# Performance work log

Hardware: AMD Instinct MI355X
Metric: run time of the kernel (lower is better)

The kernel has to match this reference:

```python
import jax, jax.numpy as jnp
import numpy as np

B = 1024
INPUT_DIM = 768
NUM_CLASSES = 5
NUM_PRIMARY_CAPS = 32
PRIMARY_CAP_DIM = 8
ROUTING_CAP_DIM = 16
NUM_ITER = 3
PROJ_DIM = 256 * 6 * 6  # 9216
NUM_IN_CAPS = NUM_PRIMARY_CAPS * 16  # conv output is 4x4 spatial -> 512


def squash(t, axis=-1):
    sq = jnp.sum(t * t, axis=axis, keepdims=True)
    scale = sq / (1.0 + sq)
    return scale * t / jnp.sqrt(sq + 1e-8)


def setup_inputs() -> dict:
    key = jax.random.key(0)
    k = jax.random.split(key, 6)
    x = jax.random.normal(k[0], (B, INPUT_DIM), dtype=jnp.float32)
    W1 = jax.random.normal(k[1], (INPUT_DIM, PROJ_DIM), dtype=jnp.float32) * 0.02
    b1 = jnp.zeros((PROJ_DIM,), dtype=jnp.float32)
    convW = jax.random.normal(k[2], (NUM_PRIMARY_CAPS * PRIMARY_CAP_DIM, 256, 3, 3), dtype=jnp.float32) * 0.02  # OIHW
    convB = jnp.zeros((NUM_PRIMARY_CAPS * PRIMARY_CAP_DIM,), dtype=jnp.float32)
    # matches torch.randn init in RoutingCapsules: [num_in, num_out, out_dim, in_dim]
    Wr = jax.random.normal(k[3], (NUM_IN_CAPS, NUM_CLASSES, ROUTING_CAP_DIM, PRIMARY_CAP_DIM), dtype=jnp.float32)
    return {"x": x, "W1": W1, "b1": b1, "convW": convW, "convB": convB, "Wr": Wr}


def reference(x, W1, b1, convW, convB, Wr):
    # feature projection (dropout is identity in eval)
    h = jax.nn.relu(x @ W1 + b1)
    h = h.reshape(-1, 256, 6, 6)
    # primary capsules conv: k=3, s=1, pad=0 -> [B, 256, 4, 4]
    out = jax.lax.conv_general_dilated(h, convW, window_strides=(1, 1), padding='VALID',
                                       dimension_numbers=('NCHW', 'OIHW', 'NCHW'))
    out = out + convB[None, :, None, None]
    bsz = out.shape[0]
    out = out.reshape(bsz, NUM_PRIMARY_CAPS, PRIMARY_CAP_DIM, -1)      # [B,32,8,16]
    out = jnp.transpose(out, (0, 1, 3, 2)).reshape(bsz, -1, PRIMARY_CAP_DIM)  # [B,512,8]
    u = squash(out, axis=-1)
    # prediction vectors u_hat: [B, in_caps, out_caps, out_dim]
    u_hat = jnp.einsum('nodi,bni->bnod', Wr, u)
    # dynamic routing
    b_logits = jnp.zeros((bsz, NUM_IN_CAPS, NUM_CLASSES, 1), dtype=u_hat.dtype)
    v = None
    for it in range(NUM_ITER):
        c = jax.nn.softmax(b_logits, axis=2)
        s = jnp.sum(c * u_hat, axis=1)  # [B, out_caps, out_dim]
        v = squash(s, axis=-1)
        if it < NUM_ITER - 1:
            agreement = jnp.sum(u_hat * v[:, None], axis=-1, keepdims=True)
            b_logits = b_logits + agreement
    class_probs = jnp.sqrt(jnp.sum(v * v, axis=-1))
    return (class_probs, v)
```

## Files before the change

### kernel.cpp

```cpp
#include <hip/hip_runtime.h>
#include <hip/hip_fp16.h>

#define BSZ   1024
#define INDIM 768
#define PROJ  9216
#define NCAP  512
#define NCLS  5
#define K2    2304

typedef __bf16    bf16x8 __attribute__((ext_vector_type(8)));
typedef _Float16  f16x8  __attribute__((ext_vector_type(8)));
typedef float     f32x4  __attribute__((ext_vector_type(4)));
typedef _Float16  h2     __attribute__((ext_vector_type(2)));

static __device__ __forceinline__ unsigned short f2bf(float f) {
  unsigned int x = __float_as_uint(f);
  return (unsigned short)((x + 0x7fffu + ((x >> 16) & 1u)) >> 16);
}
static __device__ __forceinline__ float bf2f(unsigned int u) {
  return __uint_as_float(u << 16);
}
static __device__ __forceinline__ unsigned short f2h(float f) {
  return __builtin_bit_cast(unsigned short, (_Float16)f);
}

#if defined(__has_builtin)
#if __has_builtin(__builtin_amdgcn_fdot2)
#define HAVE_FDOT2 1
#endif
#endif
static __device__ __forceinline__ float fdot2(h2 a, h2 b, float c) {
#ifdef HAVE_FDOT2
  return __builtin_amdgcn_fdot2(a, b, c, false);
#else
  return c + (float)a[0] * (float)b[0] + (float)a[1] * (float)b[1];
#endif
}
static __device__ __forceinline__ h2 u2h2(unsigned int u) {
  return __builtin_bit_cast(h2, u);
}

static __device__ __forceinline__ void gload16(const void* g, void* l) {
  auto gp = reinterpret_cast<const unsigned int __attribute__((address_space(1)))*>(
      (unsigned long long)g);
  auto lp = reinterpret_cast<unsigned int __attribute__((address_space(3)))*>(
      (unsigned long long)l);
  __builtin_amdgcn_global_load_lds(gp, lp, 16, 0, 0);
}

__global__ __launch_bounds__(256) void mfma_gemm_bk64(
    const unsigned short* __restrict__ A,
    const unsigned short* __restrict__ Bt,
    const float* __restrict__ bias,
    unsigned short* __restrict__ Cout,
    int M, int N, int K) {
  __shared__ __align__(16) unsigned short smem[32768];
  const int t    = threadIdx.x;
  const int bn   = blockIdx.x * 128;
  const int bm   = blockIdx.y * 128;
  const int lane = t & 63, wid = t >> 6;
  const int wm   = (wid >> 1) * 64;
  const int wn   = (wid & 1) * 64;
  const int l15  = lane & 15, kb = lane >> 4;

  const unsigned short* asrc[4];
  const unsigned short* bsrc[4];
#pragma unroll
  for (int cc = 0; cc < 4; ++cc) {
    const int c = t + cc * 256;
    const int row = c >> 3, seg = c & 7;
    const int sk = (seg ^ (row & 7)) << 3;
    asrc[cc] = A  + (size_t)(bm + row) * K + sk;
    bsrc[cc] = Bt + (size_t)(bn + row) * K + sk;
  }

  int aoff[4][2], boff[4][2];
#pragma unroll
  for (int i = 0; i < 4; ++i)
#pragma unroll
    for (int kk = 0; kk < 2; ++kk) {
      const int ra = wm + i * 16 + l15, sa = kk * 4 + kb;
      aoff[i][kk] = ra * 64 + ((sa ^ (ra & 7)) << 3);
      const int rb = wn + i * 16 + l15;
      boff[i][kk] = 8192 + rb * 64 + ((sa ^ (rb & 7)) << 3);
    }

  f32x4 acc[4][4];
#pragma unroll
  for (int i = 0; i < 4; ++i)
#pragma unroll
    for (int j = 0; j < 4; ++j)
#pragma unroll
      for (int q = 0; q < 4; ++q) acc[i][j][q] = 0.f;

  const int nk = K >> 6;
  auto stage = [&](int ks, int buf) {
    const int ko = ks << 6;
    unsigned short* sb = &smem[buf * 16384];
#pragma unroll
    for (int cc = 0; cc < 4; ++cc) {
      gload16(asrc[cc] + ko, sb + (t + cc * 256) * 8);
      gload16(bsrc[cc] + ko, sb + 8192 + (t + cc * 256) * 8);
    }
  };

  stage(0, 0);
  __syncthreads();

  int buf = 0;
  for (int ks = 0; ks < nk; ++ks) {
    if (ks + 1 < nk) stage(ks + 1, buf ^ 1);
    const unsigned short* base = &smem[buf * 16384];
    bf16x8 af[4][2], bfr[4][2];
#pragma unroll
    for (int i = 0; i < 4; ++i)
#pragma unroll
      for (int kk = 0; kk < 2; ++kk) {
        af[i][kk]  = *(const bf16x8*)(base + aoff[i][kk]);
        bfr[i][kk] = *(const bf16x8*)(base + boff[i][kk]);
      }
#pragma unroll
    for (int kk = 0; kk < 2; ++kk)
#pragma unroll
      for (int i = 0; i < 4; ++i)
#pragma unroll
        for (int j = 0; j < 4; ++j)
          acc[i][j] = __builtin_amdgcn_mfma_f32_16x16x32_bf16(af[i][kk], bfr[j][kk], acc[i][j], 0, 0, 0);
    __syncthreads();
    buf ^= 1;
  }

#pragma unroll
  for (int j = 0; j < 4; ++j) {
    const int col = bn + wn + j * 16 + l15;
    const float bv = bias[col];
#pragma unroll
    for (int i = 0; i < 4; ++i)
#pragma unroll
      for (int q = 0; q < 4; ++q) {
        const int row = bm + wm + i * 16 + kb * 4 + q;
        Cout[(size_t)row * N + col] = f2bf(fmaxf(acc[i][j][q] + bv, 0.f));
      }
  }
}

__global__ __launch_bounds__(256) void conv_gemm_sq128(
    const unsigned short* __restrict__ ht,
    const unsigned short* __restrict__ Wt2,
    const float* __restrict__ convB,
    unsigned short* __restrict__ U) {
  __shared__ __align__(16) unsigned short smem[32768];
  const int t    = threadIdx.x;
  const int bn   = blockIdx.x * 128;
  const int bm   = blockIdx.y * 128;
  const int lane = t & 63, wid = t >> 6;
  const int wm   = (wid >> 1) * 64;
  const int wn   = (wid & 1) * 64;
  const int l15  = lane & 15, kb = lane >> 4;

  const unsigned short* asrc[4];
  const unsigned short* bsrc[4];
#pragma unroll
  for (int cc = 0; cc < 4; ++cc) {
    const int c = t + cc * 256;
    const int row = c >> 3, seg = c & 7;
    const int gr = bm + row, b = gr >> 4, p = gr & 15;
    const int spb = (p >> 2) * 6 + (p & 3);
    asrc[cc] = ht + (size_t)b * PROJ + spb * 256 + ((seg ^ (row & 7)) << 3);
    bsrc[cc] = Wt2 + (size_t)(bn + row) * K2 + ((seg ^ (row & 7)) << 3);
  }

  int aoff[4][2], boff[4][2];
#pragma unroll
  for (int i = 0; i < 4; ++i)
#pragma unroll
    for (int kk = 0; kk < 2; ++kk) {
      const int ra = wm + i * 16 + l15, sa = kk * 4 + kb;
      aoff[i][kk] = ra * 64 + ((sa ^ (ra & 7)) << 3);
      const int rb = wn + i * 16 + l15;
      boff[i][kk] = 8192 + rb * 64 + ((sa ^ (rb & 7)) << 3);
    }

  f32x4 acc[4][4];
#pragma unroll
  for (int i = 0; i < 4; ++i)
#pragma unroll
    for (int j = 0; j < 4; ++j)
#pragma unroll
      for (int q = 0; q < 4; ++q) acc[i][j][q] = 0.f;

  auto stage = [&](int ks, int buf) {
    const int tap  = ks >> 2;
    const int aofs = (tap + 3 * (tap / 3)) * 256 + ((ks & 3) << 6);
    const int bofs = ks << 6;
    unsigned short* sb = &smem[buf * 16384];
#pragma unroll
    for (int cc = 0; cc < 4; ++cc) {
      gload16(asrc[cc] + aofs, sb + (t + cc * 256) * 8);
      gload16(bsrc[cc] + bofs, sb + 8192 + (t + cc * 256) * 8);
    }
  };

  stage(0, 0);
  __syncthreads();

  int buf = 0;
  for (int ks = 0; ks < 36; ++ks) {
    if (ks + 1 < 36) stage(ks + 1, buf ^ 1);
    const unsigned short* base = &smem[buf * 16384];
    bf16x8 af[4][2], bfr[4][2];
#pragma unroll
    for (int i = 0; i < 4; ++i)
#pragma unroll
      for (int kk = 0; kk < 2; ++kk) {
        af[i][kk]  = *(const bf16x8*)(base + aoff[i][kk]);
        bfr[i][kk] = *(const bf16x8*)(base + boff[i][kk]);
      }
#pragma unroll
    for (int kk = 0; kk < 2; ++kk)
#pragma unroll
      for (int i = 0; i < 4; ++i)
#pragma unroll
        for (int j = 0; j < 4; ++j)
          acc[i][j] = __builtin_amdgcn_mfma_f32_16x16x32_bf16(af[i][kk], bfr[j][kk], acc[i][j], 0, 0, 0);
    __syncthreads();
    buf ^= 1;
  }

#pragma unroll
  for (int j = 0; j < 4; ++j) {
    const int oc  = bn + wn + j * 16 + l15;
    const int cap = oc >> 3, ii = oc & 7;
    const float bv = convB[oc];
#pragma unroll
    for (int i = 0; i < 4; ++i)
#pragma unroll
      for (int q = 0; q < 4; ++q) {
        const int row = bm + wm + i * 16 + kb * 4 + q;
        const int b = row >> 4, p = row & 15;
        const float val = acc[i][j][q] + bv;
        float sq = val * val;
        sq += __shfl_xor(sq, 1);
        sq += __shfl_xor(sq, 2);
        sq += __shfl_xor(sq, 4);
        const float scale = sq / (1.f + sq) / sqrtf(sq + 1e-8f);
        U[(size_t)b * 4096 + cap * 128 + p * 8 + ii] = f2h(val * scale);
      }
  }
}

#define NX_ITEMS (BSZ * INDIM / 4)
#define NW_ITEMS (NCAP * 640 / 4)
#define NC_ITEMS 65536
#define NB_ITEMS PROJ
#define PREP_TOTAL (NX_ITEMS + NW_ITEMS + NC_ITEMS + NB_ITEMS)

__global__ __launch_bounds__(256) void prep_small(
    const float* __restrict__ x, unsigned short* __restrict__ xb,
    const float* __restrict__ Wr, __half2* __restrict__ wrh,
    const float* __restrict__ convW, unsigned short* __restrict__ wt2,
    const float* __restrict__ b1, float* __restrict__ pb1) {
  const int id = blockIdx.x * 256 + threadIdx.x;
  if (id < NX_ITEMS) {
    float4 v = ((const float4*)x)[id];
    ushort4 o;
    o.x = f2bf(v.x); o.y = f2bf(v.y); o.z = f2bf(v.z); o.w = f2bf(v.w);
    ((ushort4*)xb)[id] = o;
  } else if (id < NX_ITEMS + NW_ITEMS) {
    const int i = id - NX_ITEMS;
    float4 v = ((const float4*)Wr)[i];
    wrh[i * 2]     = __floats2half2_rn(v.x, v.y);
    wrh[i * 2 + 1] = __floats2half2_rn(v.z, v.w);
  } else if (id < NX_ITEMS + NW_ITEMS + NC_ITEMS) {
    const int i = id - NX_ITEMS - NW_ITEMS;
    const int oc = i >> 8, ic = i & 255;
    const float* s = convW + (size_t)i * 9;
#pragma unroll
    for (int tap = 0; tap < 9; ++tap)
      wt2[(size_t)oc * K2 + tap * 256 + ic] = f2bf(s[tap]);
  } else if (id < PREP_TOTAL) {
    const int n = id - NX_ITEMS - NW_ITEMS - NC_ITEMS;
    pb1[(n % 36) * 256 + n / 36] = b1[n];
  }
}

__global__ __launch_bounds__(256) void transpose_w1_perm(const float* __restrict__ W,
                                                         unsigned short* __restrict__ Wt) {
  __shared__ float tile[32][33];
  const int n0 = blockIdx.x * 32, k0 = blockIdx.y * 32;
  const int r = threadIdx.x >> 3, c = (threadIdx.x & 7) * 4;
  float4 v = *(const float4*)(W + (size_t)(k0 + r) * PROJ + n0 + c);
  tile[r][c] = v.x; tile[r][c + 1] = v.y; tile[r][c + 2] = v.z; tile[r][c + 3] = v.w;
  __syncthreads();
  ushort4 o;
  o.x = f2bf(tile[c + 0][r]); o.y = f2bf(tile[c + 1][r]);
  o.z = f2bf(tile[c + 2][r]); o.w = f2bf(tile[c + 3][r]);
  const int nn = n0 + r;
  const int prow = (nn % 36) * 256 + nn / 36;
  *(ushort4*)(Wt + (size_t)prow * INDIM + k0 + c) = o;
}

__global__ __launch_bounds__(512) void uhat_gemm(
    const unsigned short* __restrict__ U,
    const unsigned short* __restrict__ Wrh,
    unsigned short* __restrict__ uhat,
    float* __restrict__ s0q,
    int b0, int CB) {
  __shared__ float sred[8][16][80];
  const int mt = blockIdx.x, q = blockIdx.y;
  const int t = threadIdx.x, wid = t >> 6, lane = t & 63;
  const int l15 = lane & 15, kb = lane >> 4;
  const int bm = mt * 16;
  const int gb = b0 + bm;

  f32x4 sacc[5];
#pragma unroll
  for (int j = 0; j < 5; ++j)
#pragma unroll
    for (int r = 0; r < 4; ++r) sacc[j][r] = 0.f;

  const uint4 zz = make_uint4(0, 0, 0, 0);
#pragma unroll
  for (int i = 0; i < 8; ++i) {
    const int n = q * 64 + wid * 8 + i;
    uint4 av = zz;
    if (kb == 0) av = *(const uint4*)(U + (size_t)(gb + l15) * 4096 + n * 8);
    const f16x8 uf = __builtin_bit_cast(f16x8, av);
#pragma unroll
    for (int jn = 0; jn < 5; ++jn) {
      uint4 wv = zz;
      if (kb == 0) wv = *(const uint4*)(Wrh + (size_t)n * 640 + (jn * 16 + l15) * 8);
      f32x4 z;
      z[0] = 0.f; z[1] = 0.f; z[2] = 0.f; z[3] = 0.f;
      f32x4 c = __builtin_amdgcn_mfma_f32_16x16x32_f16(
          __builtin_bit_cast(f16x8, wv), uf, z, 0, 0, 0);
      ushort4 st;
      st.x = f2h(c[0]); st.y = f2h(c[1]); st.z = f2h(c[2]); st.w = f2h(c[3]);
      *(ushort4*)(uhat + ((size_t)(bm + l15) * 512 + n) * 80 + jn * 16 + kb * 4) = st;
#pragma unroll
      for (int qq = 0; qq < 4; ++qq) sacc[jn][qq] += c[qq];
    }
  }

#pragma unroll
  for (int jn = 0; jn < 5; ++jn)
#pragma unroll
    for (int qq = 0; qq < 4; ++qq)
      sred[wid][l15][jn * 16 + kb * 4 + qq] = sacc[jn][qq];
  __syncthreads();
#pragma unroll
  for (int k = 0; k < 3; ++k) {
    const int id = t + k * 512;
    if (id < 1280) {
      const int bb = id / 80, od = id % 80;
      float val = 0.f;
#pragma unroll
      for (int w = 0; w < 8; ++w) val += sred[w][bb][od];
      s0q[((size_t)q * CB + bm + bb) * 80 + od] = val;
    }
  }
}

template <int MODE>
__global__ __launch_bounds__(256) void route_pass(
    const unsigned short* __restrict__ uhat,
    const float* __restrict__ s0q,
    const float* __restrict__ vsum_in,
    float* __restrict__ vsum_out,
    float* __restrict__ out,
    int b0, int CB) {
  __shared__ unsigned int vph2[40];
  __shared__ float red[4][2][40];
  const int bl = blockIdx.x;
  const int b  = b0 + bl;
  const int t  = threadIdx.x;

  float v0r = 0.f;
  if (t < 80) {
    if (MODE == 1) {
      float s = 0.f;
#pragma unroll
      for (int g = 0; g < 8; ++g) s += s0q[((size_t)g * CB + bl) * 80 + t];
      s *= 0.2f;
      float sq = s * s;
      sq += __shfl_xor(sq, 1);
      sq += __shfl_xor(sq, 2);
      sq += __shfl_xor(sq, 4);
      sq += __shfl_xor(sq, 8);
      const float scale = sq / (1.f + sq) / sqrtf(sq + 1e-8f);
      v0r = s * scale;
    } else {
      v0r = vsum_in[(size_t)bl * 80 + t];
    }
    const float vnext = __shfl_down(v0r, 1);
    if ((t & 1) == 0)
      vph2[t >> 1] = __builtin_bit_cast(unsigned int, __floats2half2_rn(v0r, vnext));
  }
  __syncthreads();

  const int p = t >> 1, h = t & 1;
  float acc[5][8];
#pragma unroll
  for (int o = 0; o < 5; ++o)
#pragma unroll
    for (int j = 0; j < 8; ++j) acc[o][j] = 0.f;

  const unsigned short* ub = uhat + (size_t)bl * 40960;
  for (int c4 = 0; c4 < 4; ++c4) {
    const int n = c4 * 128 + p;
    const unsigned short* row = ub + n * 80 + h * 8;
    uint4 uv[5];
#pragma unroll
    for (int o = 0; o < 5; ++o) uv[o] = *(const uint4*)(row + o * 16);
    float ap[5];
#pragma unroll
    for (int o = 0; o < 5; ++o) {
      const int vb = o * 8 + h * 4;
      float a = fdot2(u2h2(uv[o].x), u2h2(vph2[vb]), 0.f);
      a = fdot2(u2h2(uv[o].y), u2h2(vph2[vb + 1]), a);
      a = fdot2(u2h2(uv[o].z), u2h2(vph2[vb + 2]), a);
      a = fdot2(u2h2(uv[o].w), u2h2(vph2[vb + 3]), a);
      ap[o] = a + __shfl_xor(a, 1);
    }
    float m = ap[0];
#pragma unroll
    for (int o = 1; o < 5; ++o) m = fmaxf(m, ap[o]);
    float es = 0.f, e[5];
#pragma unroll
    for (int o = 0; o < 5; ++o) { e[o] = __expf(ap[o] - m); es += e[o]; }
    const float inv = 1.f / es;
#pragma unroll
    for (int o = 0; o < 5; ++o) {
      const float cc = e[o] * inv;
      h2 hx = u2h2(uv[o].x), hy = u2h2(uv[o].y), hz = u2h2(uv[o].z), hw = u2h2(uv[o].w);
      acc[o][0] += cc * (float)hx[0]; acc[o][1] += cc * (float)hx[1];
      acc[o][2] += cc * (float)hy[0]; acc[o][3] += cc * (float)hy[1];
      acc[o][4] += cc * (float)hz[0]; acc[o][5] += cc * (float)hz[1];
      acc[o][6] += cc * (float)hw[0]; acc[o][7] += cc * (float)hw[1];
    }
  }

#pragma unroll
  for (int off = 2; off <= 32; off <<= 1)
#pragma unroll
    for (int o = 0; o < 5; ++o)
#pragma unroll
      for (int j = 0; j < 8; ++j) acc[o][j] += __shfl_xor(acc[o][j], off);
  const int wid = t >> 6, lane = t & 63;
  if (lane < 2) {
#pragma unroll
    for (int o = 0; o < 5; ++o)
#pragma unroll
      for (int j = 0; j < 8; ++j) red[wid][lane][o * 8 + j] = acc[o][j];
  }
  __syncthreads();

  if (t < 80) {
    const int o = t >> 4, d = t & 15, hh = d >> 3, dl = d & 7;
    const int c = o * 8 + dl;
    float s = red[0][hh][c] + red[1][hh][c] + red[2][hh][c] + red[3][hh][c];
    float sq = s * s;
    sq += __shfl_xor(sq, 1);
    sq += __shfl_xor(sq, 2);
    sq += __shfl_xor(sq, 4);
    sq += __shfl_xor(sq, 8);
    const float scale = sq / (1.f + sq) / sqrtf(sq + 1e-8f);
    const float vn = s * scale;
    if (MODE == 1) {
      vsum_out[(size_t)bl * 80 + t] = v0r + vn;
    } else {
      out[5 * BSZ + (size_t)b * 80 + t] = vn;
      float vv = vn * vn;
      vv += __shfl_xor(vv, 1);
      vv += __shfl_xor(vv, 2);
      vv += __shfl_xor(vv, 4);
      vv += __shfl_xor(vv, 8);
      if ((t & 15) == 0) out[(size_t)b * 5 + o] = sqrtf(vv);
    }
  }
}

extern "C" void kernel_launch(void* const* d_in, const int* in_sizes, int n_in,
                              void* d_out, int out_size, void* d_ws, size_t ws_size,
                              hipStream_t stream) {
  const float* x     = (const float*)d_in[0];
  const float* W1    = (const float*)d_in[1];
  const float* b1    = (const float*)d_in[2];
  const float* convW = (const float*)d_in[3];
  const float* convB = (const float*)d_in[4];
  const float* Wr    = (const float*)d_in[5];
  float* out = (float*)d_out;

  char* base = (char*)d_ws;
  size_t off = 0;
  auto alloc = [&](size_t bytes) { size_t o = off; off = (off + bytes + 255) & ~(size_t)255; return o; };
  const size_t o_wrh  = alloc((size_t)NCAP * 640 * 2);
  const size_t o_u    = alloc((size_t)BSZ * 4096 * 2);
  const size_t o_s0q  = alloc((size_t)8 * BSZ * 80 * 4);
  const size_t o_vsum = alloc((size_t)BSZ * 80 * 4);
  const size_t o_pool = off;
  size_t poff = o_pool;
  auto palloc = [&](size_t bytes) { size_t o = poff; poff = (poff + bytes + 255) & ~(size_t)255; return o; };
  const size_t o_ht  = palloc((size_t)BSZ * PROJ * 2);
  const size_t o_w1t = palloc((size_t)PROJ * INDIM * 2);
  const size_t o_xb  = palloc((size_t)BSZ * INDIM * 2);
  const size_t o_wt2 = palloc((size_t)256 * K2 * 2);
  const size_t o_pb1 = palloc((size_t)PROJ * 4);

  unsigned short* ht   = (unsigned short*)(base + o_ht);
  unsigned short* w1t  = (unsigned short*)(base + o_w1t);
  unsigned short* xb   = (unsigned short*)(base + o_xb);
  unsigned short* wt2  = (unsigned short*)(base + o_wt2);
  float*          pb1  = (float*)(base + o_pb1);
  unsigned short* wrh  = (unsigned short*)(base + o_wrh);
  unsigned short* u    = (unsigned short*)(base + o_u);
  float*          s0q  = (float*)(base + o_s0q);
  float*          vsum = (float*)(base + o_vsum);
  unsigned short* uhat = (unsigned short*)(base + o_pool);

  prep_small<<<(PREP_TOTAL + 255) / 256, 256, 0, stream>>>(
      x, xb, Wr, (__half2*)wrh, convW, wt2, b1, pb1);
  transpose_w1_perm<<<dim3(PROJ / 32, INDIM / 32), 256, 0, stream>>>(W1, w1t);

  mfma_gemm_bk64<<<dim3(PROJ / 128, BSZ / 128), 256, 0, stream>>>(
      xb, w1t, pb1, ht, BSZ, PROJ, INDIM);

  conv_gemm_sq128<<<dim3(2, 128), 256, 0, stream>>>(ht, wt2, convB, u);

  const size_t pool_sz = ws_size > o_pool ? ws_size - o_pool : 0;
  int CB = 1024;
  while (CB > 16 && (size_t)CB * 512 * 80 * 2 > pool_sz) CB >>= 1;
  for (int b0 = 0; b0 < BSZ; b0 += CB) {
    uhat_gemm<<<dim3(CB / 16, 8), 512, 0, stream>>>(u, wrh, uhat, s0q, b0, CB);
    route_pass<1><<<CB, 256, 0, stream>>>(uhat, s0q, nullptr, vsum, out, b0, CB);
    route_pass<2><<<CB, 256, 0, stream>>>(uhat, nullptr, vsum, nullptr, out, b0, CB);
  }
}
```

Before: 157.0 us.

## Precompute routing iteration 0 via weight-summed GEMM and fuse iteration 1 into uhat

Adds a small GEMM that computes s0 directly from u and a transposed fp16 copy of Wr, exploiting uniform softmax at iteration 0, giving v0 before u_hat exists. The u_hat kernel then computes iteration 1 agreement and softmax inline, so one full pass over u_hat (route_pass<1>) is removed. The W1 transpose is merged into the prep kernel to save a launch. The conv GEMM tile is shrunk to 64 rows for more blocks. In exchange the uhat kernel does extra shuffles and exps, and a new v01 reduction kernel is launched.

```diff
diff --git a/kernel.cpp b/kernel.cpp
--- a/kernel.cpp
+++ b/kernel.cpp
@@ -16,9 +16,6 @@
 static __device__ __forceinline__ unsigned short f2bf(float f) {
   unsigned int x = __float_as_uint(f);
   return (unsigned short)((x + 0x7fffu + ((x >> 16) & 1u)) >> 16);
-}
-static __device__ __forceinline__ float bf2f(unsigned int u) {
-  return __uint_as_float(u << 16);
 }
 static __device__ __forceinline__ unsigned short f2h(float f) {
   return __builtin_bit_cast(unsigned short, (_Float16)f);
@@ -144,48 +141,56 @@
   }
 }
 
-__global__ __launch_bounds__(256) void conv_gemm_sq128(
+__global__ __launch_bounds__(256) void conv_gemm_sq(
     const unsigned short* __restrict__ ht,
     const unsigned short* __restrict__ Wt2,
     const float* __restrict__ convB,
     unsigned short* __restrict__ U) {
-  __shared__ __align__(16) unsigned short smem[32768];
+  __shared__ __align__(16) unsigned short smem[24576];
   const int t    = threadIdx.x;
   const int bn   = blockIdx.x * 128;
-  const int bm   = blockIdx.y * 128;
+  const int bm   = blockIdx.y * 64;
   const int lane = t & 63, wid = t >> 6;
-  const int wm   = (wid >> 1) * 64;
-  const int wn   = (wid & 1) * 64;
   const int l15  = lane & 15, kb = lane >> 4;
 
-  const unsigned short* asrc[4];
-  const unsigned short* bsrc[4];
-#pragma unroll
-  for (int cc = 0; cc < 4; ++cc) {
+  const unsigned short* asrc[2];
+#pragma unroll
+  for (int cc = 0; cc < 2; ++cc) {
     const int c = t + cc * 256;
     const int row = c >> 3, seg = c & 7;
     const int gr = bm + row, b = gr >> 4, p = gr & 15;
     const int spb = (p >> 2) * 6 + (p & 3);
     asrc[cc] = ht + (size_t)b * PROJ + spb * 256 + ((seg ^ (row & 7)) << 3);
+  }
+  const unsigned short* bsrc[4];
+#pragma unroll
+  for (int cc = 0; cc < 4; ++cc) {
+    const int c = t + cc * 256;
+    const int row = c >> 3, seg = c & 7;
     bsrc[cc] = Wt2 + (size_t)(bn + row) * K2 + ((seg ^ (row & 7)) << 3);
   }
 
-  int aoff[4][2], boff[4][2];
+  int aoff[4][2], boff[2][2];
 #pragma unroll
   for (int i = 0; i < 4; ++i)
 #pragma unroll
     for (int kk = 0; kk < 2; ++kk) {
-      const int ra = wm + i * 16 + l15, sa = kk * 4 + kb;
-      aoff[i][kk] = ra * 64 + ((sa ^ (ra & 7)) << 3);
-      const int rb = wn + i * 16 + l15;
-      boff[i][kk] = 8192 + rb * 64 + ((sa ^ (rb & 7)) << 3);
-    }
-
-  f32x4 acc[4][4];
+      const int row = i * 16 + l15, seg = kk * 4 + kb;
+      aoff[i][kk] = row * 64 + ((seg ^ (row & 7)) << 3);
+    }
+#pragma unroll
+  for (int j = 0; j < 2; ++j)
+#pragma unroll
+    for (int kk = 0; kk < 2; ++kk) {
+      const int row = wid * 32 + j * 16 + l15, seg = kk * 4 + kb;
+      boff[j][kk] = 4096 + row * 64 + ((seg ^ (row & 7)) << 3);
+    }
+
+  f32x4 acc[4][2];
 #pragma unroll
   for (int i = 0; i < 4; ++i)
 #pragma unroll
-    for (int j = 0; j < 4; ++j)
+    for (int j = 0; j < 2; ++j)
 #pragma unroll
       for (int q = 0; q < 4; ++q) acc[i][j][q] = 0.f;
 
@@ -193,12 +198,13 @@
     const int tap  = ks >> 2;
     const int aofs = (tap + 3 * (tap / 3)) * 256 + ((ks & 3) << 6);
     const int bofs = ks << 6;
-    unsigned short* sb = &smem[buf * 16384];
-#pragma unroll
-    for (int cc = 0; cc < 4; ++cc) {
-      gload16(asrc[cc] + aofs, sb + (t + cc * 256) * 8);
-      gload16(bsrc[cc] + bofs, sb + 8192 + (t + cc * 256) * 8);
-    }
+    unsigned short* sb = &smem[buf * 12288];
+    gload16(asrc[0] + aofs, sb + t * 8);
+    gload16(asrc[1] + aofs, sb + t * 8 + 2048);
+    gload16(bsrc[0] + bofs, sb + 4096 + t * 8);
+    gload16(bsrc[1] + bofs, sb + 4096 + t * 8 + 2048);
+    gload16(bsrc[2] + bofs, sb + 4096 + t * 8 + 4096);
+    gload16(bsrc[3] + bofs, sb + 4096 + t * 8 + 6144);
   };
 
   stage(0, 0);
@@ -207,36 +213,37 @@
   int buf = 0;
   for (int ks = 0; ks < 36; ++ks) {
     if (ks + 1 < 36) stage(ks + 1, buf ^ 1);
-    const unsigned short* base = &smem[buf * 16384];
-    bf16x8 af[4][2], bfr[4][2];
+    const unsigned short* base = &smem[buf * 12288];
+    bf16x8 af[4][2], bfr[2][2];
 #pragma unroll
     for (int i = 0; i < 4; ++i)
 #pragma unroll
-      for (int kk = 0; kk < 2; ++kk) {
-        af[i][kk]  = *(const bf16x8*)(base + aoff[i][kk]);
-        bfr[i][kk] = *(const bf16x8*)(base + boff[i][kk]);
-      }
+      for (int kk = 0; kk < 2; ++kk) af[i][kk] = *(const bf16x8*)(base + aoff[i][kk]);
+#pragma unroll
+    for (int j = 0; j < 2; ++j)
+#pragma unroll
+      for (int kk = 0; kk < 2; ++kk) bfr[j][kk] = *(const bf16x8*)(base + boff[j][kk]);
 #pragma unroll
     for (int kk = 0; kk < 2; ++kk)
 #pragma unroll
       for (int i = 0; i < 4; ++i)
 #pragma unroll
-        for (int j = 0; j < 4; ++j)
+        for (int j = 0; j < 2; ++j)
           acc[i][j] = __builtin_amdgcn_mfma_f32_16x16x32_bf16(af[i][kk], bfr[j][kk], acc[i][j], 0, 0, 0);
     __syncthreads();
     buf ^= 1;
   }
 
 #pragma unroll
-  for (int j = 0; j < 4; ++j) {
-    const int oc  = bn + wn + j * 16 + l15;
+  for (int j = 0; j < 2; ++j) {
+    const int oc  = bn + wid * 32 + j * 16 + l15;
     const int cap = oc >> 3, ii = oc & 7;
     const float bv = convB[oc];
 #pragma unroll
-    for (int i = 0; i < 4; ++i)
+    for (int i = 0; i < 4; ++i) {
 #pragma unroll
       for (int q = 0; q < 4; ++q) {
-        const int row = bm + wm + i * 16 + kb * 4 + q;
+        const int row = bm + i * 16 + kb * 4 + q;
         const int b = row >> 4, p = row & 15;
         const float val = acc[i][j][q] + bv;
         float sq = val * val;
@@ -246,21 +253,43 @@
         const float scale = sq / (1.f + sq) / sqrtf(sq + 1e-8f);
         U[(size_t)b * 4096 + cap * 128 + p * 8 + ii] = f2h(val * scale);
       }
-  }
-}
-
+    }
+  }
+}
+
+#define TP_BLOCKS (288 * 24)
 #define NX_ITEMS (BSZ * INDIM / 4)
 #define NW_ITEMS (NCAP * 640 / 4)
+#define NWT_ITEMS (NCAP * 80)
 #define NC_ITEMS 65536
 #define NB_ITEMS PROJ
-#define PREP_TOTAL (NX_ITEMS + NW_ITEMS + NC_ITEMS + NB_ITEMS)
-
-__global__ __launch_bounds__(256) void prep_small(
+#define EW_TOTAL (NX_ITEMS + NW_ITEMS + NWT_ITEMS + NC_ITEMS + NB_ITEMS)
+#define EW_BLOCKS (EW_TOTAL / 256)
+
+__global__ __launch_bounds__(256) void prep_all(
+    const float* __restrict__ W1, unsigned short* __restrict__ w1t,
     const float* __restrict__ x, unsigned short* __restrict__ xb,
     const float* __restrict__ Wr, __half2* __restrict__ wrh,
+    unsigned short* __restrict__ wrh_t,
     const float* __restrict__ convW, unsigned short* __restrict__ wt2,
     const float* __restrict__ b1, float* __restrict__ pb1) {
-  const int id = blockIdx.x * 256 + threadIdx.x;
+  __shared__ float tile[32][33];
+  if (blockIdx.x < TP_BLOCKS) {
+    const int tb = blockIdx.x;
+    const int n0 = (tb % 288) * 32, k0 = (tb / 288) * 32;
+    const int r = threadIdx.x >> 3, c = (threadIdx.x & 7) * 4;
+    float4 v = *(const float4*)(W1 + (size_t)(k0 + r) * PROJ + n0 + c);
+    tile[r][c] = v.x; tile[r][c + 1] = v.y; tile[r][c + 2] = v.z; tile[r][c + 3] = v.w;
+    __syncthreads();
+    ushort4 o;
+    o.x = f2bf(tile[c + 0][r]); o.y = f2bf(tile[c + 1][r]);
+    o.z = f2bf(tile[c + 2][r]); o.w = f2bf(tile[c + 3][r]);
+    const int nn = n0 + r;
+    const int prow = (nn % 36) * 256 + nn / 36;
+    *(ushort4*)(w1t + (size_t)prow * INDIM + k0 + c) = o;
+    return;
+  }
+  const int id = (blockIdx.x - TP_BLOCKS) * 256 + threadIdx.x;
   if (id < NX_ITEMS) {
     float4 v = ((const float4*)x)[id];
     ushort4 o;
@@ -271,40 +300,78 @@
     float4 v = ((const float4*)Wr)[i];
     wrh[i * 2]     = __floats2half2_rn(v.x, v.y);
     wrh[i * 2 + 1] = __floats2half2_rn(v.z, v.w);
-  } else if (id < NX_ITEMS + NW_ITEMS + NC_ITEMS) {
+  } else if (id < NX_ITEMS + NW_ITEMS + NWT_ITEMS) {
     const int i = id - NX_ITEMS - NW_ITEMS;
+    const int od = i / NCAP, n = i % NCAP;
+    const float4 a = *(const float4*)(Wr + (size_t)n * 640 + od * 8);
+    const float4 b = *(const float4*)(Wr + (size_t)n * 640 + od * 8 + 4);
+    __half2 h0 = __floats2half2_rn(a.x, a.y), h1 = __floats2half2_rn(a.z, a.w);
+    __half2 h2v = __floats2half2_rn(b.x, b.y), h3 = __floats2half2_rn(b.z, b.w);
+    uint4 st = make_uint4(__builtin_bit_cast(unsigned int, h0),
+                          __builtin_bit_cast(unsigned int, h1),
+                          __builtin_bit_cast(unsigned int, h2v),
+                          __builtin_bit_cast(unsigned int, h3));
+    *(uint4*)(wrh_t + (size_t)od * 4096 + n * 8) = st;
+  } else if (id < NX_ITEMS + NW_ITEMS + NWT_ITEMS + NC_ITEMS) {
+    const int i = id - NX_ITEMS - NW_ITEMS - NWT_ITEMS;
     const int oc = i >> 8, ic = i & 255;
     const float* s = convW + (size_t)i * 9;
 #pragma unroll
     for (int tap = 0; tap < 9; ++tap)
       wt2[(size_t)oc * K2 + tap * 256 + ic] = f2bf(s[tap]);
-  } else if (id < PREP_TOTAL) {
-    const int n = id - NX_ITEMS - NW_ITEMS - NC_ITEMS;
+  } else if (id < EW_TOTAL) {
+    const int n = id - NX_ITEMS - NW_ITEMS - NWT_ITEMS - NC_ITEMS;
     pb1[(n % 36) * 256 + n / 36] = b1[n];
   }
 }
 
-__global__ __launch_bounds__(256) void transpose_w1_perm(const float* __restrict__ W,
-                                                         unsigned short* __restrict__ Wt) {
-  __shared__ float tile[32][33];
-  const int n0 = blockIdx.x * 32, k0 = blockIdx.y * 32;
-  const int r = threadIdx.x >> 3, c = (threadIdx.x & 7) * 4;
-  float4 v = *(const float4*)(W + (size_t)(k0 + r) * PROJ + n0 + c);
-  tile[r][c] = v.x; tile[r][c + 1] = v.y; tile[r][c + 2] = v.z; tile[r][c + 3] = v.w;
-  __syncthreads();
-  ushort4 o;
-  o.x = f2bf(tile[c + 0][r]); o.y = f2bf(tile[c + 1][r]);
-  o.z = f2bf(tile[c + 2][r]); o.w = f2bf(tile[c + 3][r]);
-  const int nn = n0 + r;
-  const int prow = (nn % 36) * 256 + nn / 36;
-  *(ushort4*)(Wt + (size_t)prow * INDIM + k0 + c) = o;
-}
-
-__global__ __launch_bounds__(512) void uhat_gemm(
+__global__ __launch_bounds__(256) void s0v0_gemm(
+    const unsigned short* __restrict__ U,
+    const unsigned short* __restrict__ WrhT,
+    float* __restrict__ v0) {
+  __shared__ float red[4][16][16];
+  __shared__ float sl[16][17];
+  __shared__ float scl[16];
+  const int bt = blockIdx.x, o = blockIdx.y;
+  const int t = threadIdx.x, wid = t >> 6, lane = t & 63;
+  const int l15 = lane & 15, kb = lane >> 4;
+  const int gb = bt * 16;
+
+  f32x4 acc;
+  acc[0] = 0.f; acc[1] = 0.f; acc[2] = 0.f; acc[3] = 0.f;
+  const unsigned short* abase = WrhT + (size_t)(o * 16 + l15) * 4096 + kb * 8;
+  const unsigned short* bbase = U + (size_t)(gb + l15) * 4096 + kb * 8;
+  const int k0b = wid * 1024;
+#pragma unroll 4
+  for (int k0 = k0b; k0 < k0b + 1024; k0 += 32) {
+    const f16x8 av = __builtin_bit_cast(f16x8, *(const uint4*)(abase + k0));
+    const f16x8 bv = __builtin_bit_cast(f16x8, *(const uint4*)(bbase + k0));
+    acc = __builtin_amdgcn_mfma_f32_16x16x32_f16(av, bv, acc, 0, 0, 0);
+  }
+#pragma unroll
+  for (int q = 0; q < 4; ++q) red[wid][kb * 4 + q][l15] = acc[q];
+  __syncthreads();
+  const int row = t >> 4, col = t & 15;
+  const float s = 0.2f * (red[0][row][col] + red[1][row][col] +
+                          red[2][row][col] + red[3][row][col]);
+  sl[row][col] = s;
+  __syncthreads();
+  if (t < 16) {
+    float sq = 0.f;
+#pragma unroll
+    for (int r = 0; r < 16; ++r) { const float xx = sl[r][t]; sq += xx * xx; }
+    scl[t] = sq / (1.f + sq) / sqrtf(sq + 1e-8f);
+  }
+  __syncthreads();
+  v0[(size_t)(gb + col) * 80 + o * 16 + row] = s * scl[col];
+}
+
+__global__ __launch_bounds__(512) void uhat_p1(
     const unsigned short* __restrict__ U,
     const unsigned short* __restrict__ Wrh,
+    const float* __restrict__ v0,
     unsigned short* __restrict__ uhat,
-    float* __restrict__ s0q,
+    float* __restrict__ sp1,
     int b0, int CB) {
   __shared__ float sred[8][16][80];
   const int mt = blockIdx.x, q = blockIdx.y;
@@ -313,11 +380,16 @@
   const int bm = mt * 16;
   const int gb = b0 + bm;
 
+  f32x4 vreg[5];
+#pragma unroll
+  for (int jn = 0; jn < 5; ++jn)
+    vreg[jn] = *(const f32x4*)(v0 + (size_t)(gb + l15) * 80 + jn * 16 + kb * 4);
+
   f32x4 sacc[5];
 #pragma unroll
-  for (int j = 0; j < 5; ++j)
-#pragma unroll
-    for (int r = 0; r < 4; ++r) sacc[j][r] = 0.f;
+  for (int jn = 0; jn < 5; ++jn)
+#pragma unroll
+    for (int qq = 0; qq < 4; ++qq) sacc[jn][qq] = 0.f;
 
   const uint4 zz = make_uint4(0, 0, 0, 0);
 #pragma unroll
@@ -326,19 +398,39 @@
     uint4 av = zz;
     if (kb == 0) av = *(const uint4*)(U + (size_t)(gb + l15) * 4096 + n * 8);
     const f16x8 uf = __builtin_bit_cast(f16x8, av);
+    f32x4 cfr[5];
 #pragma unroll
     for (int jn = 0; jn < 5; ++jn) {
       uint4 wv = zz;
       if (kb == 0) wv = *(const uint4*)(Wrh + (size_t)n * 640 + (jn * 16 + l15) * 8);
       f32x4 z;
       z[0] = 0.f; z[1] = 0.f; z[2] = 0.f; z[3] = 0.f;
-      f32x4 c = __builtin_amdgcn_mfma_f32_16x16x32_f16(
+      cfr[jn] = __builtin_amdgcn_mfma_f32_16x16x32_f16(
           __builtin_bit_cast(f16x8, wv), uf, z, 0, 0, 0);
       ushort4 st;
-      st.x = f2h(c[0]); st.y = f2h(c[1]); st.z = f2h(c[2]); st.w = f2h(c[3]);
+      st.x = f2h(cfr[jn][0]); st.y = f2h(cfr[jn][1]);
+      st.z = f2h(cfr[jn][2]); st.w = f2h(cfr[jn][3]);
       *(ushort4*)(uhat + ((size_t)(bm + l15) * 512 + n) * 80 + jn * 16 + kb * 4) = st;
-#pragma unroll
-      for (int qq = 0; qq < 4; ++qq) sacc[jn][qq] += c[qq];
+    }
+    float a[5];
+#pragma unroll
+    for (int jn = 0; jn < 5; ++jn) {
+      float d = cfr[jn][0] * vreg[jn][0] + cfr[jn][1] * vreg[jn][1] +
+                cfr[jn][2] * vreg[jn][2] + cfr[jn][3] * vreg[jn][3];
+      d += __shfl_xor(d, 16);
+      d += __shfl_xor(d, 32);
+      a[jn] = d;
+    }
+    float m = fmaxf(fmaxf(fmaxf(a[0], a[1]), fmaxf(a[2], a[3])), a[4]);
+    float c[5], es = 0.f;
+#pragma unroll
+    for (int o = 0; o < 5; ++o) { c[o] = __expf(a[o] - m); es += c[o]; }
+    const float inv = 1.f / es;
+#pragma unroll
+    for (int jn = 0; jn < 5; ++jn) {
+      const float cc = c[jn] * inv;
+#pragma unroll
+      for (int qq = 0; qq < 4; ++qq) sacc[jn][qq] += cc * cfr[jn][qq];
     }
   }
 
@@ -356,19 +448,33 @@
       float val = 0.f;
 #pragma unroll
       for (int w = 0; w < 8; ++w) val += sred[w][bb][od];
-      s0q[((size_t)q * CB + bm + bb) * 80 + od] = val;
-    }
-  }
-}
-
-template <int MODE>
-__global__ __launch_bounds__(256) void route_pass(
+      sp1[((size_t)q * BSZ + gb + bb) * 80 + od] = val;
+    }
+  }
+}
+
+__global__ __launch_bounds__(128) void v01_k(
+    const float* __restrict__ sp1, const float* __restrict__ v0,
+    float* __restrict__ v01, int b0) {
+  const int b = b0 + blockIdx.x, t = threadIdx.x;
+  if (t < 80) {
+    float s = 0.f;
+#pragma unroll
+    for (int g = 0; g < 8; ++g) s += sp1[((size_t)g * BSZ + b) * 80 + t];
+    float sq = s * s;
+    sq += __shfl_xor(sq, 1);
+    sq += __shfl_xor(sq, 2);
+    sq += __shfl_xor(sq, 4);
+    sq += __shfl_xor(sq, 8);
+    const float scale = sq / (1.f + sq) / sqrtf(sq + 1e-8f);
+    v01[(size_t)b * 80 + t] = v0[(size_t)b * 80 + t] + s * scale;
+  }
+}
+
+__global__ __launch_bounds__(256) void route_pass2(
     const unsigned short* __restrict__ uhat,
-    const float* __restrict__ s0q,
     const float* __restrict__ vsum_in,
-    float* __restrict__ vsum_out,
-    float* __restrict__ out,
-    int b0, int CB) {
+    float* __restrict__ out, int b0) {
   __shared__ unsigned int vph2[40];
   __shared__ float red[4][2][40];
   const int bl = blockIdx.x;
@@ -377,21 +483,7 @@
 
   float v0r = 0.f;
   if (t < 80) {
-    if (MODE == 1) {
-      float s = 0.f;
-#pragma unroll
-      for (int g = 0; g < 8; ++g) s += s0q[((size_t)g * CB + bl) * 80 + t];
-      s *= 0.2f;
-      float sq = s * s;
-      sq += __shfl_xor(sq, 1);
-      sq += __shfl_xor(sq, 2);
-      sq += __shfl_xor(sq, 4);
-      sq += __shfl_xor(sq, 8);
-      const float scale = sq / (1.f + sq) / sqrtf(sq + 1e-8f);
-      v0r = s * scale;
-    } else {
-      v0r = vsum_in[(size_t)bl * 80 + t];
-    }
+    v0r = vsum_in[(size_t)b * 80 + t];
     const float vnext = __shfl_down(v0r, 1);
     if ((t & 1) == 0)
       vph2[t >> 1] = __builtin_bit_cast(unsigned int, __floats2half2_rn(v0r, vnext));
@@ -466,17 +558,13 @@
     sq += __shfl_xor(sq, 8);
     const float scale = sq / (1.f + sq) / sqrtf(sq + 1e-8f);
     const float vn = s * scale;
-    if (MODE == 1) {
-      vsum_out[(size_t)bl * 80 + t] = v0r + vn;
-    } else {
-      out[5 * BSZ + (size_t)b * 80 + t] = vn;
-      float vv = vn * vn;
-      vv += __shfl_xor(vv, 1);
-      vv += __shfl_xor(vv, 2);
-      vv += __shfl_xor(vv, 4);
-      vv += __shfl_xor(vv, 8);
-      if ((t & 15) == 0) out[(size_t)b * 5 + o] = sqrtf(vv);
-    }
+    out[5 * BSZ + (size_t)b * 80 + t] = vn;
+    float vv = vn * vn;
+    vv += __shfl_xor(vv, 1);
+    vv += __shfl_xor(vv, 2);
+    vv += __shfl_xor(vv, 4);
+    vv += __shfl_xor(vv, 8);
+    if ((t & 15) == 0) out[(size_t)b * 5 + o] = sqrtf(vv);
   }
 }
 
@@ -495,9 +583,11 @@
   size_t off = 0;
   auto alloc = [&](size_t bytes) { size_t o = off; off = (off + bytes + 255) & ~(size_t)255; return o; };
   const size_t o_wrh  = alloc((size_t)NCAP * 640 * 2);
+  const size_t o_wrt  = alloc((size_t)80 * 4096 * 2);
   const size_t o_u    = alloc((size_t)BSZ * 4096 * 2);
-  const size_t o_s0q  = alloc((size_t)8 * BSZ * 80 * 4);
-  const size_t o_vsum = alloc((size_t)BSZ * 80 * 4);
+  const size_t o_sp1  = alloc((size_t)8 * BSZ * 80 * 4);
+  const size_t o_v0   = alloc((size_t)BSZ * 80 * 4);
+  const size_t o_v01  = alloc((size_t)BSZ * 80 * 4);
   const size_t o_pool = off;
   size_t poff = o_pool;
   auto palloc = [&](size_t bytes) { size_t o = poff; poff = (poff + bytes + 255) & ~(size_t)255; return o; };
@@ -513,26 +603,29 @@
   unsigned short* wt2  = (unsigned short*)(base + o_wt2);
   float*          pb1  = (float*)(base + o_pb1);
   unsigned short* wrh  = (unsigned short*)(base + o_wrh);
+  unsigned short* wrt  = (unsigned short*)(base + o_wrt);
   unsigned short* u    = (unsigned short*)(base + o_u);
-  float*          s0q  = (float*)(base + o_s0q);
-  float*          vsum = (float*)(base + o_vsum);
+  float*          sp1  = (float*)(base + o_sp1);
+  float*          v0   = (float*)(base + o_v0);
+  float*          v01  = (float*)(base + o_v01);
   unsigned short* uhat = (unsigned short*)(base + o_pool);
 
-  prep_small<<<(PREP_TOTAL + 255) / 256, 256, 0, stream>>>(
-      x, xb, Wr, (__half2*)wrh, convW, wt2, b1, pb1);
-  transpose_w1_perm<<<dim3(PROJ / 32, INDIM / 32), 256, 0, stream>>>(W1, w1t);
+  prep_all<<<TP_BLOCKS + EW_BLOCKS, 256, 0, stream>>>(
+      W1, w1t, x, xb, Wr, (__half2*)wrh, wrt, convW, wt2, b1, pb1);
 
   mfma_gemm_bk64<<<dim3(PROJ / 128, BSZ / 128), 256, 0, stream>>>(
       xb, w1t, pb1, ht, BSZ, PROJ, INDIM);
 
-  conv_gemm_sq128<<<dim3(2, 128), 256, 0, stream>>>(ht, wt2, convB, u);
+  conv_gemm_sq<<<dim3(2, 256), 256, 0, stream>>>(ht, wt2, convB, u);
+
+  s0v0_gemm<<<dim3(BSZ / 16, 5), 256, 0, stream>>>(u, wrt, v0);
 
   const size_t pool_sz = ws_size > o_pool ? ws_size - o_pool : 0;
   int CB = 1024;
   while (CB > 16 && (size_t)CB * 512 * 80 * 2 > pool_sz) CB >>= 1;
   for (int b0 = 0; b0 < BSZ; b0 += CB) {
-    uhat_gemm<<<dim3(CB / 16, 8), 512, 0, stream>>>(u, wrh, uhat, s0q, b0, CB);
-    route_pass<1><<<CB, 256, 0, stream>>>(uhat, s0q, nullptr, vsum, out, b0, CB);
-    route_pass<2><<<CB, 256, 0, stream>>>(uhat, nullptr, vsum, nullptr, out, b0, CB);
-  }
-}
+    uhat_p1<<<dim3(CB / 16, 8), 512, 0, stream>>>(u, wrh, v0, uhat, sp1, b0, CB);
+    v01_k<<<CB, 128, 0, stream>>>(sp1, v0, v01, b0);
+    route_pass2<<<CB, 256, 0, stream>>>(uhat, v01, out, b0);
+  }
+}
```

Result: faster. 152.4 us (-2.9%).
